# Optimization experiments

Hardware: AMD Instinct MI355X
Metric: run time of the kernel (lower is better)

Reference implementation:

```python
import jax, jax.numpy as jnp
import numpy as np

N_NODES = 100000
N_EDGES = 1600000
IN_F = 128
OUT_F = 32


def setup_inputs() -> dict:
    key = jax.random.key(0)
    k1, k2, k3, k4, k5 = jax.random.split(key, 5)
    x = jax.random.normal(k1, (N_NODES, IN_F), dtype=jnp.float32)
    edge_row = jax.random.randint(k2, (N_EDGES,), 0, N_NODES, dtype=jnp.int64 if jax.config.jax_enable_x64 else jnp.int32)
    edge_col = jax.random.randint(k3, (N_EDGES,), 0, N_NODES, dtype=jnp.int64 if jax.config.jax_enable_x64 else jnp.int32)
    edge_val = jax.random.uniform(k4, (N_EDGES,), dtype=jnp.float32)
    # Xavier-normal init like nn.init.xavier_normal_
    std = float(np.sqrt(2.0 / (IN_F + OUT_F)))
    weight = jax.random.normal(k5, (IN_F, OUT_F), dtype=jnp.float32) * std
    bias = jnp.zeros((OUT_F,), dtype=jnp.float32)
    return {"x": x, "edge_row": edge_row, "edge_col": edge_col,
            "edge_val": edge_val, "weight": weight, "bias": bias}


def reference(x, edge_row, edge_col, edge_val, weight, bias):
    # support = x @ W  (dense GEMM)
    support = x @ weight  # [N, out]
    # output = adj @ support, adj in COO form: out[row] += val * support[col]
    gathered = support[edge_col] * edge_val[:, None]  # [E, out]
    output = jax.ops.segment_sum(gathered, edge_row, num_segments=N_NODES)
    return output + bias
```

## Files before the change

kernel.cpp:

```cpp
#include <hip/hip_runtime.h>
#include <hip/hip_bf16.h>

#define N_NODES 100000
#define N_EDGES 1600000
#define IN_F 128
#define OUT_F 32

#define NBK 782
#define CAP 2816
#define TILE_A 6144
#define NWG_A 261
#define NWG_G 98
#define OVCAP 4096

typedef float v4f __attribute__((ext_vector_type(4)));
typedef short bf16x8 __attribute__((ext_vector_type(8)));
typedef float f32x4 __attribute__((ext_vector_type(4)));

__device__ inline unsigned short f2bf(float f) {
  unsigned u = __float_as_uint(f);
  return (unsigned short)((u + 0x7FFFu + ((u >> 16) & 1u)) >> 16);
}
__device__ inline float bf2f(unsigned short h) {
  return __uint_as_float(((unsigned)h) << 16);
}
__device__ inline unsigned pk2(float lo, float hi) {
  return (unsigned)f2bf(lo) | ((unsigned)f2bf(hi) << 16);
}

__global__ __launch_bounds__(1024) void gcn_fused_kernel(
    const float* __restrict__ x, const float* __restrict__ w,
    unsigned short* __restrict__ sup, const int* __restrict__ erow,
    const int* __restrict__ ecol, const float* __restrict__ eval,
    int* __restrict__ cursor, int* __restrict__ ovcnt, int4* __restrict__ ov,
    int2* __restrict__ bedges) {
  __shared__ int h[NBK];
  __shared__ int gbase[NBK];
  __shared__ int lcur[NBK];
  const int t = threadIdx.x;

  if (blockIdx.x < NWG_G) {
    const int wid = t >> 6;
    const int lane = t & 63;
    const int lr = lane & 15;
    const int lg = lane >> 4;
    const int wrow0 = blockIdx.x * 1024 + wid * 64;

    bf16x8 bfrag[2][4];
    #pragma unroll
    for (int nt = 0; nt < 2; ++nt) {
      #pragma unroll
      for (int kk = 0; kk < 4; ++kk) {
        const int c = nt * 16 + lr;
        const int k0 = kk * 32 + lg * 8;
        union { unsigned u[4]; bf16x8 v; } bf;
        #pragma unroll
        for (int d = 0; d < 4; ++d)
          bf.u[d] = pk2(w[(k0 + 2 * d) * OUT_F + c],
                        w[(k0 + 2 * d + 1) * OUT_F + c]);
        bfrag[nt][kk] = bf.v;
      }
    }

    f32x4 acc[4][2];
    #pragma unroll
    for (int m = 0; m < 4; ++m) { acc[m][0] = 0.f; acc[m][1] = 0.f; }

    #pragma unroll
    for (int m = 0; m < 4; ++m) {
      const int row = wrow0 + m * 16 + lr;
      const int rl = (row < N_NODES) ? row : (N_NODES - 1);
      const float* xr = x + (size_t)rl * IN_F;
      #pragma unroll
      for (int kk = 0; kk < 4; ++kk) {
        const v4f p0 = *(const v4f*)(xr + kk * 32 + lg * 8);
        const v4f p1 = *(const v4f*)(xr + kk * 32 + lg * 8 + 4);
        union { unsigned u[4]; bf16x8 v; } af;
        af.u[0] = pk2(p0.x, p0.y);
        af.u[1] = pk2(p0.z, p0.w);
        af.u[2] = pk2(p1.x, p1.y);
        af.u[3] = pk2(p1.z, p1.w);
        acc[m][0] = __builtin_amdgcn_mfma_f32_16x16x32_bf16(af.v, bfrag[0][kk], acc[m][0], 0, 0, 0);
        acc[m][1] = __builtin_amdgcn_mfma_f32_16x16x32_bf16(af.v, bfrag[1][kk], acc[m][1], 0, 0, 0);
      }
    }
    #pragma unroll
    for (int m = 0; m < 4; ++m) {
      #pragma unroll
      for (int i = 0; i < 4; ++i) {
        const int r = wrow0 + m * 16 + lg * 4 + i;
        if (r < N_NODES) {
          sup[((size_t)r << 5) + lr] = f2bf(acc[m][0][i]);
          sup[((size_t)r << 5) + 16 + lr] = f2bf(acc[m][1][i]);
        }
      }
    }
  } else {
    const int base = (blockIdx.x - NWG_G) * TILE_A;
    for (int i = t; i < NBK; i += 1024) { h[i] = 0; lcur[i] = 0; }
    __syncthreads();
    int rowv[6];
    #pragma unroll
    for (int i = 0; i < 6; ++i) {
      const int e = base + i * 1024 + t;
      rowv[i] = (e < N_EDGES) ? erow[e] : -1;
      if (rowv[i] >= 0) atomicAdd(&h[rowv[i] >> 7], 1);
    }
    __syncthreads();
    if (t < NBK) {
      const int c = h[t];
      gbase[t] = c ? atomicAdd(&cursor[t], (c + 3) & ~3) : 0;
    }
    __syncthreads();
    #pragma unroll
    for (int i = 0; i < 6; ++i) {
      if (rowv[i] >= 0) {
        const int e = base + i * 1024 + t;
        const int r = rowv[i];
        const int b = r >> 7;
        const int k = atomicAdd(&lcur[b], 1);
        const int pos = gbase[b] + k;
        const int2 pk = make_int2(ecol[e] | ((r & 127) << 17),
                                  __float_as_int(eval[e]));
        if (pos < CAP) {
          bedges[(size_t)b * CAP + pos] = pk;
        } else {
          const int o = atomicAdd(ovcnt, 1);
          if (o < OVCAP) ov[o] = make_int4(b, pk.x, pk.y, 0);
        }
      }
    }
    __syncthreads();
    if (t < NBK) {
      const int c = h[t];
      const int resv = (c + 3) & ~3;
      for (int j = c; j < resv; ++j) {
        const int pos = gbase[t] + j;
        if (pos < CAP) bedges[(size_t)t * CAP + pos] = make_int2(0, 0);
      }
    }
  }
}

__global__ __launch_bounds__(1024) void gcn_gather_kernel(
    const unsigned short* __restrict__ sup, const int* __restrict__ cursor,
    const int2* __restrict__ bedges, const int* __restrict__ ovcnt,
    const int4* __restrict__ ov, const float* __restrict__ bias,
    float* __restrict__ out) {
  __shared__ int2 stage[CAP];
  __shared__ int2 sorted[CAP];
  __shared__ int hist[128];
  __shared__ int csr[129];
  __shared__ int cur[128];
  const int t = threadIdx.x;
  const int b = blockIdx.x;
  const int f = t & 31;
  const int g = t >> 5;
  const int ext = min(cursor[b], CAP);
  const size_t bb = (size_t)b * CAP;
  float acc[4] = {0.f, 0.f, 0.f, 0.f};

  if (t < 128) hist[t] = 0;
  __syncthreads();
  for (int j = t; j < ext; j += 1024) {
    const int2 ed = bedges[bb + j];
    stage[j] = ed;
    if (ed.y != 0) atomicAdd(&hist[(ed.x >> 17) & 127], 1);
  }
  __syncthreads();
  if (t < 64) {
    const int v0 = hist[2 * t];
    const int v1 = hist[2 * t + 1];
    int s = v0 + v1;
    #pragma unroll
    for (int off = 1; off < 64; off <<= 1) {
      const int up = __shfl_up(s, off, 64);
      if (t >= off) s += up;
    }
    const int excl = s - (v0 + v1);
    csr[2 * t] = excl;
    csr[2 * t + 1] = excl + v0;
    cur[2 * t] = excl;
    cur[2 * t + 1] = excl + v0;
    if (t == 63) csr[128] = s;
  }
  __syncthreads();
  for (int j = t; j < ext; j += 1024) {
    const int2 ed = stage[j];
    if (ed.y != 0) {
      const int k = atomicAdd(&cur[(ed.x >> 17) & 127], 1);
      sorted[k] = ed;
    }
  }
  __syncthreads();

  #pragma unroll
  for (int rr = 0; rr < 4; ++rr) {
    const int lr = g * 4 + rr;
    const int e1 = csr[lr + 1];
    int e = csr[lr];
    for (; e + 8 <= e1; e += 8) {
      const int2 q0 = sorted[e],     q1 = sorted[e + 1];
      const int2 q2 = sorted[e + 2], q3 = sorted[e + 3];
      const int2 q4 = sorted[e + 4], q5 = sorted[e + 5];
      const int2 q6 = sorted[e + 6], q7 = sorted[e + 7];
      const float v0 = bf2f(sup[((size_t)(q0.x & 0x1FFFF) << 5) + f]);
      const float v1 = bf2f(sup[((size_t)(q1.x & 0x1FFFF) << 5) + f]);
      const float v2 = bf2f(sup[((size_t)(q2.x & 0x1FFFF) << 5) + f]);
      const float v3 = bf2f(sup[((size_t)(q3.x & 0x1FFFF) << 5) + f]);
      const float v4 = bf2f(sup[((size_t)(q4.x & 0x1FFFF) << 5) + f]);
      const float v5 = bf2f(sup[((size_t)(q5.x & 0x1FFFF) << 5) + f]);
      const float v6 = bf2f(sup[((size_t)(q6.x & 0x1FFFF) << 5) + f]);
      const float v7 = bf2f(sup[((size_t)(q7.x & 0x1FFFF) << 5) + f]);
      acc[rr] += __int_as_float(q0.y) * v0 + __int_as_float(q1.y) * v1 +
                 __int_as_float(q2.y) * v2 + __int_as_float(q3.y) * v3 +
                 __int_as_float(q4.y) * v4 + __int_as_float(q5.y) * v5 +
                 __int_as_float(q6.y) * v6 + __int_as_float(q7.y) * v7;
    }
    for (; e + 4 <= e1; e += 4) {
      const int2 q0 = sorted[e],     q1 = sorted[e + 1];
      const int2 q2 = sorted[e + 2], q3 = sorted[e + 3];
      const float v0 = bf2f(sup[((size_t)(q0.x & 0x1FFFF) << 5) + f]);
      const float v1 = bf2f(sup[((size_t)(q1.x & 0x1FFFF) << 5) + f]);
      const float v2 = bf2f(sup[((size_t)(q2.x & 0x1FFFF) << 5) + f]);
      const float v3 = bf2f(sup[((size_t)(q3.x & 0x1FFFF) << 5) + f]);
      acc[rr] += __int_as_float(q0.y) * v0 + __int_as_float(q1.y) * v1 +
                 __int_as_float(q2.y) * v2 + __int_as_float(q3.y) * v3;
    }
    for (; e < e1; ++e) {
      const int2 q = sorted[e];
      acc[rr] += __int_as_float(q.y) *
                 bf2f(sup[((size_t)(q.x & 0x1FFFF) << 5) + f]);
    }
  }

  const int on = min(*ovcnt, OVCAP);
  for (int i = 0; i < on; ++i) {
    const int4 q = ov[i];
    if (q.x == b) {
      const int lr = (q.y >> 17) & 127;
      if ((lr >> 2) == g)
        acc[lr & 3] += __int_as_float(q.z) *
                       bf2f(sup[((size_t)(q.y & 0x1FFFF) << 5) + f]);
    }
  }

  const int row0 = b << 7;
  const float bv = bias[f];
  #pragma unroll
  for (int rr = 0; rr < 4; ++rr) {
    const int row = row0 + g * 4 + rr;
    if (row < N_NODES) out[((size_t)row << 5) + f] = acc[rr] + bv;
  }
}

__global__ __launch_bounds__(256) void gcn_gemm_fb_kernel(
    const float* __restrict__ x, const float* __restrict__ w,
    unsigned short* __restrict__ sup) {
  __shared__ float wlds[IN_F][OUT_F];
  const int t = threadIdx.x;
  for (int i = t; i < 1024; i += 256)
    ((float4*)wlds)[i] = ((const float4*)w)[i];
  __syncthreads();
  const int tr = t >> 3;
  const int c0 = (t & 7) * 4;
  const int row = blockIdx.x * 32 + tr;
  if (row >= N_NODES) return;
  const float* xr = x + (size_t)row * IN_F;
  v4f acc = 0.f;
  #pragma unroll 4
  for (int kb = 0; kb < IN_F; kb += 4) {
    const v4f xv = *(const v4f*)(xr + kb);
    acc += xv.x * *(const v4f*)&wlds[kb + 0][c0];
    acc += xv.y * *(const v4f*)&wlds[kb + 1][c0];
    acc += xv.z * *(const v4f*)&wlds[kb + 2][c0];
    acc += xv.w * *(const v4f*)&wlds[kb + 3][c0];
  }
  ushort4 o;
  o.x = f2bf(acc.x); o.y = f2bf(acc.y); o.z = f2bf(acc.z); o.w = f2bf(acc.w);
  *(ushort4*)(sup + ((size_t)row << 5) + c0) = o;
}

__global__ __launch_bounds__(256) void gcn_init_out_kernel(
    float* __restrict__ out, const float* __restrict__ bias) {
  const int i = blockIdx.x * 256 + threadIdx.x;
  if (i < N_NODES * OUT_F / 4)
    ((float4*)out)[i] = ((const float4*)bias)[i & 7];
}

__global__ __launch_bounds__(256) void gcn_scatter_kernel(
    const unsigned short* __restrict__ sup, const int* __restrict__ erow,
    const int* __restrict__ ecol, const float* __restrict__ eval,
    float* __restrict__ out) {
  const long long idx = (long long)blockIdx.x * 256 + threadIdx.x;
  if (idx >= (long long)N_EDGES * OUT_F) return;
  const int e = (int)(idx >> 5);
  const int ff = (int)(idx & 31);
  atomicAdd(&out[((size_t)erow[e] << 5) + ff],
            eval[e] * bf2f(sup[((size_t)ecol[e] << 5) + ff]));
}

extern "C" void kernel_launch(void* const* d_in, const int* in_sizes, int n_in,
                              void* d_out, int out_size, void* d_ws, size_t ws_size,
                              hipStream_t stream) {
  const float* x = (const float*)d_in[0];
  const int* erow = (const int*)d_in[1];
  const int* ecol = (const int*)d_in[2];
  const float* eval = (const float*)d_in[3];
  const float* w = (const float*)d_in[4];
  const float* bias = (const float*)d_in[5];
  float* out = (float*)d_out;
  char* ws = (char*)d_ws;

  const size_t SUP_OFF = 0;
  const size_t CUR_OFF = SUP_OFF + 6400000;
  const size_t OVC_OFF = CUR_OFF + 3128;
  const size_t OV_OFF  = CUR_OFF + 3200;
  const size_t BED_OFF = OV_OFF + 65536;
  const size_t NEEDED  = BED_OFF + (size_t)NBK * CAP * 8;

  unsigned short* sup = (unsigned short*)(ws + SUP_OFF);

  if (ws_size >= NEEDED) {
    int* cursor = (int*)(ws + CUR_OFF);
    int* ovcnt  = (int*)(ws + OVC_OFF);
    int4* ov    = (int4*)(ws + OV_OFF);
    int2* bedges = (int2*)(ws + BED_OFF);

    hipMemsetAsync(cursor, 0, 3132, stream);
    gcn_fused_kernel<<<NWG_G + NWG_A, 1024, 0, stream>>>(
        x, w, sup, erow, ecol, eval, cursor, ovcnt, ov, bedges);
    gcn_gather_kernel<<<NBK, 1024, 0, stream>>>(
        sup, cursor, bedges, ovcnt, ov, bias, out);
  } else if (ws_size >= 6400000) {
    gcn_gemm_fb_kernel<<<(N_NODES + 31) / 32, 256, 0, stream>>>(x, w, sup);
    gcn_init_out_kernel<<<(N_NODES * OUT_F / 4 + 255) / 256, 256, 0, stream>>>(out, bias);
    const long long total = (long long)N_EDGES * OUT_F;
    gcn_scatter_kernel<<<(int)((total + 255) / 256), 256, 0, stream>>>(
        sup, erow, ecol, eval, out);
  }
}
```

Before: 68.61 us.

## Split fused GEMM/bucketing kernel into separate launches with LDS-staged GEMM

The fused kernel, which ran the GEMM and the edge bucketing in different workgroups of one launch, is split into two kernels launched back to back. The new GEMM uses 256-thread blocks of 128 rows: it stages x into LDS as bf16 with coalesced loads, then reads MFMA fragments from LDS, replacing strided per-lane global loads. This is meant to improve memory coalescing and occupancy for the GEMM, at the cost of an extra launch and losing the overlap between GEMM and bucketing.

```diff
diff --git a/kernel.cpp b/kernel.cpp
--- a/kernel.cpp
+++ b/kernel.cpp
@@ -10,7 +10,6 @@
 #define CAP 2816
 #define TILE_A 6144
 #define NWG_A 261
-#define NWG_G 98
 #define OVCAP 4096
 
 typedef float v4f __attribute__((ext_vector_type(4)));
@@ -28,116 +27,121 @@
   return (unsigned)f2bf(lo) | ((unsigned)f2bf(hi) << 16);
 }
 
-__global__ __launch_bounds__(1024) void gcn_fused_kernel(
+__global__ __launch_bounds__(256) void gcn_gemm_kernel(
     const float* __restrict__ x, const float* __restrict__ w,
-    unsigned short* __restrict__ sup, const int* __restrict__ erow,
-    const int* __restrict__ ecol, const float* __restrict__ eval,
-    int* __restrict__ cursor, int* __restrict__ ovcnt, int4* __restrict__ ov,
-    int2* __restrict__ bedges) {
+    unsigned short* __restrict__ sup) {
+  __shared__ unsigned short xs[128][136];
+  const int t = threadIdx.x;
+  const int row0 = blockIdx.x * 128;
+
+  const int wid = t >> 6;
+  const int lane = t & 63;
+  const int lr = lane & 15;
+  const int lg = lane >> 4;
+  bf16x8 bfrag[2][4];
+  #pragma unroll
+  for (int nt = 0; nt < 2; ++nt) {
+    #pragma unroll
+    for (int kk = 0; kk < 4; ++kk) {
+      const int c = nt * 16 + lr;
+      const int k0 = kk * 32 + lg * 8;
+      union { unsigned u[4]; bf16x8 v; } bf;
+      #pragma unroll
+      for (int d = 0; d < 4; ++d)
+        bf.u[d] = pk2(w[(k0 + 2 * d) * OUT_F + c],
+                      w[(k0 + 2 * d + 1) * OUT_F + c]);
+      bfrag[nt][kk] = bf.v;
+    }
+  }
+
+  #pragma unroll
+  for (int i = 0; i < 16; ++i) {
+    const int idx = i * 256 + t;
+    const int r = idx >> 5;
+    const int c4 = idx & 31;
+    const int row = row0 + r;
+    const int rl = (row < N_NODES) ? row : (N_NODES - 1);
+    const v4f v = *(const v4f*)(x + (size_t)rl * IN_F + c4 * 4);
+    ushort4 o;
+    o.x = f2bf(v.x); o.y = f2bf(v.y); o.z = f2bf(v.z); o.w = f2bf(v.w);
+    *(ushort4*)&xs[r][c4 * 4] = o;
+  }
+  __syncthreads();
+
+  f32x4 acc[2][2];
+  acc[0][0] = 0.f; acc[0][1] = 0.f; acc[1][0] = 0.f; acc[1][1] = 0.f;
+  #pragma unroll
+  for (int m = 0; m < 2; ++m) {
+    const int ar = wid * 32 + m * 16 + lr;
+    #pragma unroll
+    for (int kk = 0; kk < 4; ++kk) {
+      const bf16x8 afrag = *(const bf16x8*)&xs[ar][kk * 32 + lg * 8];
+      acc[m][0] = __builtin_amdgcn_mfma_f32_16x16x32_bf16(afrag, bfrag[0][kk], acc[m][0], 0, 0, 0);
+      acc[m][1] = __builtin_amdgcn_mfma_f32_16x16x32_bf16(afrag, bfrag[1][kk], acc[m][1], 0, 0, 0);
+    }
+  }
+  #pragma unroll
+  for (int m = 0; m < 2; ++m) {
+    #pragma unroll
+    for (int i = 0; i < 4; ++i) {
+      const int r = row0 + wid * 32 + m * 16 + lg * 4 + i;
+      if (r < N_NODES) {
+        sup[((size_t)r << 5) + lr] = f2bf(acc[m][0][i]);
+        sup[((size_t)r << 5) + 16 + lr] = f2bf(acc[m][1][i]);
+      }
+    }
+  }
+}
+
+__global__ __launch_bounds__(1024) void gcn_bucket_kernel(
+    const int* __restrict__ erow, const int* __restrict__ ecol,
+    const float* __restrict__ eval, int* __restrict__ cursor,
+    int* __restrict__ ovcnt, int4* __restrict__ ov, int2* __restrict__ bedges) {
   __shared__ int h[NBK];
   __shared__ int gbase[NBK];
   __shared__ int lcur[NBK];
   const int t = threadIdx.x;
-
-  if (blockIdx.x < NWG_G) {
-    const int wid = t >> 6;
-    const int lane = t & 63;
-    const int lr = lane & 15;
-    const int lg = lane >> 4;
-    const int wrow0 = blockIdx.x * 1024 + wid * 64;
-
-    bf16x8 bfrag[2][4];
-    #pragma unroll
-    for (int nt = 0; nt < 2; ++nt) {
-      #pragma unroll
-      for (int kk = 0; kk < 4; ++kk) {
-        const int c = nt * 16 + lr;
-        const int k0 = kk * 32 + lg * 8;
-        union { unsigned u[4]; bf16x8 v; } bf;
-        #pragma unroll
-        for (int d = 0; d < 4; ++d)
-          bf.u[d] = pk2(w[(k0 + 2 * d) * OUT_F + c],
-                        w[(k0 + 2 * d + 1) * OUT_F + c]);
-        bfrag[nt][kk] = bf.v;
+  const int base = blockIdx.x * TILE_A;
+  for (int i = t; i < NBK; i += 1024) { h[i] = 0; lcur[i] = 0; }
+  __syncthreads();
+  int rowv[6];
+  #pragma unroll
+  for (int i = 0; i < 6; ++i) {
+    const int e = base + i * 1024 + t;
+    rowv[i] = (e < N_EDGES) ? erow[e] : -1;
+    if (rowv[i] >= 0) atomicAdd(&h[rowv[i] >> 7], 1);
+  }
+  __syncthreads();
+  if (t < NBK) {
+    const int c = h[t];
+    gbase[t] = c ? atomicAdd(&cursor[t], (c + 3) & ~3) : 0;
+  }
+  __syncthreads();
+  #pragma unroll
+  for (int i = 0; i < 6; ++i) {
+    if (rowv[i] >= 0) {
+      const int e = base + i * 1024 + t;
+      const int r = rowv[i];
+      const int b = r >> 7;
+      const int k = atomicAdd(&lcur[b], 1);
+      const int pos = gbase[b] + k;
+      const int2 pk = make_int2(ecol[e] | ((r & 127) << 17),
+                                __float_as_int(eval[e]));
+      if (pos < CAP) {
+        bedges[(size_t)b * CAP + pos] = pk;
+      } else {
+        const int o = atomicAdd(ovcnt, 1);
+        if (o < OVCAP) ov[o] = make_int4(b, pk.x, pk.y, 0);
       }
     }
-
-    f32x4 acc[4][2];
-    #pragma unroll
-    for (int m = 0; m < 4; ++m) { acc[m][0] = 0.f; acc[m][1] = 0.f; }
-
-    #pragma unroll
-    for (int m = 0; m < 4; ++m) {
-      const int row = wrow0 + m * 16 + lr;
-      const int rl = (row < N_NODES) ? row : (N_NODES - 1);
-      const float* xr = x + (size_t)rl * IN_F;
-      #pragma unroll
-      for (int kk = 0; kk < 4; ++kk) {
-        const v4f p0 = *(const v4f*)(xr + kk * 32 + lg * 8);
-        const v4f p1 = *(const v4f*)(xr + kk * 32 + lg * 8 + 4);
-        union { unsigned u[4]; bf16x8 v; } af;
-        af.u[0] = pk2(p0.x, p0.y);
-        af.u[1] = pk2(p0.z, p0.w);
-        af.u[2] = pk2(p1.x, p1.y);
-        af.u[3] = pk2(p1.z, p1.w);
-        acc[m][0] = __builtin_amdgcn_mfma_f32_16x16x32_bf16(af.v, bfrag[0][kk], acc[m][0], 0, 0, 0);
-        acc[m][1] = __builtin_amdgcn_mfma_f32_16x16x32_bf16(af.v, bfrag[1][kk], acc[m][1], 0, 0, 0);
-      }
-    }
-    #pragma unroll
-    for (int m = 0; m < 4; ++m) {
-      #pragma unroll
-      for (int i = 0; i < 4; ++i) {
-        const int r = wrow0 + m * 16 + lg * 4 + i;
-        if (r < N_NODES) {
-          sup[((size_t)r << 5) + lr] = f2bf(acc[m][0][i]);
-          sup[((size_t)r << 5) + 16 + lr] = f2bf(acc[m][1][i]);
-        }
-      }
-    }
-  } else {
-    const int base = (blockIdx.x - NWG_G) * TILE_A;
-    for (int i = t; i < NBK; i += 1024) { h[i] = 0; lcur[i] = 0; }
-    __syncthreads();
-    int rowv[6];
-    #pragma unroll
-    for (int i = 0; i < 6; ++i) {
-      const int e = base + i * 1024 + t;
-      rowv[i] = (e < N_EDGES) ? erow[e] : -1;
-      if (rowv[i] >= 0) atomicAdd(&h[rowv[i] >> 7], 1);
-    }
-    __syncthreads();
-    if (t < NBK) {
-      const int c = h[t];
-      gbase[t] = c ? atomicAdd(&cursor[t], (c + 3) & ~3) : 0;
-    }
-    __syncthreads();
-    #pragma unroll
-    for (int i = 0; i < 6; ++i) {
-      if (rowv[i] >= 0) {
-        const int e = base + i * 1024 + t;
-        const int r = rowv[i];
-        const int b = r >> 7;
-        const int k = atomicAdd(&lcur[b], 1);
-        const int pos = gbase[b] + k;
-        const int2 pk = make_int2(ecol[e] | ((r & 127) << 17),
-                                  __float_as_int(eval[e]));
-        if (pos < CAP) {
-          bedges[(size_t)b * CAP + pos] = pk;
-        } else {
-          const int o = atomicAdd(ovcnt, 1);
-          if (o < OVCAP) ov[o] = make_int4(b, pk.x, pk.y, 0);
-        }
-      }
-    }
-    __syncthreads();
-    if (t < NBK) {
-      const int c = h[t];
-      const int resv = (c + 3) & ~3;
-      for (int j = c; j < resv; ++j) {
-        const int pos = gbase[t] + j;
-        if (pos < CAP) bedges[(size_t)t * CAP + pos] = make_int2(0, 0);
-      }
+  }
+  __syncthreads();
+  if (t < NBK) {
+    const int c = h[t];
+    const int resv = (c + 3) & ~3;
+    for (int j = c; j < resv; ++j) {
+      const int pos = gbase[t] + j;
+      if (pos < CAP) bedges[(size_t)t * CAP + pos] = make_int2(0, 0);
     }
   }
 }
@@ -254,33 +258,6 @@
   }
 }
 
-__global__ __launch_bounds__(256) void gcn_gemm_fb_kernel(
-    const float* __restrict__ x, const float* __restrict__ w,
-    unsigned short* __restrict__ sup) {
-  __shared__ float wlds[IN_F][OUT_F];
-  const int t = threadIdx.x;
-  for (int i = t; i < 1024; i += 256)
-    ((float4*)wlds)[i] = ((const float4*)w)[i];
-  __syncthreads();
-  const int tr = t >> 3;
-  const int c0 = (t & 7) * 4;
-  const int row = blockIdx.x * 32 + tr;
-  if (row >= N_NODES) return;
-  const float* xr = x + (size_t)row * IN_F;
-  v4f acc = 0.f;
-  #pragma unroll 4
-  for (int kb = 0; kb < IN_F; kb += 4) {
-    const v4f xv = *(const v4f*)(xr + kb);
-    acc += xv.x * *(const v4f*)&wlds[kb + 0][c0];
-    acc += xv.y * *(const v4f*)&wlds[kb + 1][c0];
-    acc += xv.z * *(const v4f*)&wlds[kb + 2][c0];
-    acc += xv.w * *(const v4f*)&wlds[kb + 3][c0];
-  }
-  ushort4 o;
-  o.x = f2bf(acc.x); o.y = f2bf(acc.y); o.z = f2bf(acc.z); o.w = f2bf(acc.w);
-  *(ushort4*)(sup + ((size_t)row << 5) + c0) = o;
-}
-
 __global__ __launch_bounds__(256) void gcn_init_out_kernel(
     float* __restrict__ out, const float* __restrict__ bias) {
   const int i = blockIdx.x * 256 + threadIdx.x;
@@ -328,12 +305,13 @@
     int2* bedges = (int2*)(ws + BED_OFF);
 
     hipMemsetAsync(cursor, 0, 3132, stream);
-    gcn_fused_kernel<<<NWG_G + NWG_A, 1024, 0, stream>>>(
-        x, w, sup, erow, ecol, eval, cursor, ovcnt, ov, bedges);
+    gcn_bucket_kernel<<<NWG_A, 1024, 0, stream>>>(
+        erow, ecol, eval, cursor, ovcnt, ov, bedges);
+    gcn_gemm_kernel<<<NBK, 256, 0, stream>>>(x, w, sup);
     gcn_gather_kernel<<<NBK, 1024, 0, stream>>>(
         sup, cursor, bedges, ovcnt, ov, bias, out);
   } else if (ws_size >= 6400000) {
-    gcn_gemm_fb_kernel<<<(N_NODES + 31) / 32, 256, 0, stream>>>(x, w, sup);
+    gcn_gemm_kernel<<<NBK, 256, 0, stream>>>(x, w, sup);
     gcn_init_out_kernel<<<(N_NODES * OUT_F / 4 + 255) / 256, 256, 0, stream>>>(out, bias);
     const long long total = (long long)N_EDGES * OUT_F;
     gcn_scatter_kernel<<<(int)((total + 255) / 256), 256, 0, stream>>>(
```

Result: slower. 80.35 us (+17.1%).
